# Performance work log

Measured on AMD Instinct MI355X. Metric: run time of the kernel, lower is better.

Reference implementation:

```python
import jax, jax.numpy as jnp
import numpy as np

B, T, R, NS = 16, 2048, 256, 4


def setup_inputs() -> dict:
    key = jax.random.key(0)
    ks = jax.random.split(key, 11)
    s = 1.0 / np.sqrt(R)
    inp = {
        "q": jax.random.normal(ks[0], (B, T, R), jnp.float32),
        "k": jax.random.normal(ks[1], (B, T, R), jnp.float32),
        "v": jax.random.normal(ks[2], (B, T, R), jnp.float32),
        "wq": jax.random.uniform(ks[3], (R, R), jnp.float32, -s, s),
        "bq": jax.random.uniform(ks[4], (R,), jnp.float32, -s, s),
        "wk": jax.random.uniform(ks[5], (R, R), jnp.float32, -s, s),
        "bk": jax.random.uniform(ks[6], (R,), jnp.float32, -s, s),
        "wv": jax.random.uniform(ks[7], (NS, R, R), jnp.float32, -s, s),
        "bv": jax.random.uniform(ks[8], (NS, R), jnp.float32, -s, s),
        "wp": jax.random.uniform(ks[9], (R,), jnp.float32, -s, s),
        "bp": jax.random.uniform(ks[10], (), jnp.float32, -s, s),
    }
    return inp


def reference(q, k, v, wq, bq, wk, bk, wv, bv, wp, bp):
    # linear projections (torch Linear: x @ W.T + b)
    qp = q @ wq.T + bq                                   # [B,T,R]
    kp = k @ wk.T + bk                                   # [B,T,R]
    # n_state value projections, stacked on dim 1 -> [B,NS,T,R]
    vs = jnp.einsum('btr,nor->bnto', v, wv) + bv[None, :, None, :]

    # scaled dot-product attention with tril + (score==0 -> -10000) mask quirk
    scale = 1.0 / jnp.sqrt(jnp.asarray(q.shape[-1], qp.dtype))
    score = jnp.einsum('btr,bsr->bts', qp, kp) * scale   # [B,T,T]
    score = jnp.tril(score)
    score = jnp.where(score == 0, jnp.asarray(-10000.0, score.dtype), score)
    attn = jax.nn.softmax(score, axis=-1)                # [B,T,T]

    # batched AV (original does a python loop over batch; same math)
    out = jnp.einsum('bts,bnsr->bntr', attn, vs)         # [B,NS,T,R]

    # similarity loss: 0.5 * sum |cov(proj_score[b])| averaged over batch
    proj = jnp.einsum('bntr,r->bnt', vs, wp) + bp        # [B,NS,T]

    def cov_abs_sum(X):  # X: [NS, T], rows = variables
        Xc = X - X.mean(axis=1, keepdims=True)
        c = (Xc @ Xc.T) / (X.shape[1] - 1)               # [NS,NS]
        return 0.5 * jnp.sum(jnp.abs(c))

    sim_loss = jnp.mean(jax.vmap(cov_abs_sum)(proj))
    return out, sim_loss
```

## Files before the change

kernel.cpp:

```cpp
#include <hip/hip_runtime.h>

#define B_  16
#define T_  2048
#define R_  256
#define NS_ 4

typedef unsigned short u16;
typedef __attribute__((ext_vector_type(8))) __bf16 bf16x8;
typedef __attribute__((ext_vector_type(4))) float f32x4;

__device__ __forceinline__ u16 f2bf(float f){
  union { float f; unsigned u; } x; x.f = f;
  unsigned r = x.u + 0x7FFFu + ((x.u >> 16) & 1u);
  return (u16)(r >> 16);
}
__device__ __forceinline__ float bf2f(u16 h){
  union { unsigned u; float f; } x; x.u = ((unsigned)h) << 16; return x.f;
}

__device__ __forceinline__ void async_cp16(const void* g, void* l){
  __builtin_amdgcn_global_load_lds((__attribute__((address_space(1))) void*)g,
                                   (__attribute__((address_space(3))) void*)l,
                                   16, 0, 0);
}

__global__ __launch_bounds__(256)
void cvt_kernel(const float* __restrict__ src, u16* __restrict__ dst, int n4){
  int i = blockIdx.x*256 + threadIdx.x;
  if (i >= n4) return;
  float4 f = ((const float4*)src)[i];
  ushort4 o;
  o.x = f2bf(f.x); o.y = f2bf(f.y); o.z = f2bf(f.z); o.w = f2bf(f.w);
  ((ushort4*)dst)[i] = o;
}

__global__ __launch_bounds__(256)
void zero_kernel(float* __restrict__ p, int n){
  int i = blockIdx.x*256 + threadIdx.x;
  if (i < n) p[i] = 0.0f;
}

__global__ __launch_bounds__(256, 2)
void gemm_nt_bias(const u16* __restrict__ A, const u16* __restrict__ Bm,
                  u16* __restrict__ C, const float* __restrict__ bias,
                  int lda, int ldb, int ldc, int K,
                  long long sAn, long long sBb, long long sCz,
                  int sBiasN, int biasMode)
{
  __shared__ __align__(16) u16 As[128*32];
  __shared__ __align__(16) u16 Bs[128*32];
  int tid = threadIdx.x;
  int lane = tid & 63, wave = tid >> 6;
  int z = blockIdx.z;
  int nIdx = z & 3, bIdx = z >> 2;
  A    += (long long)nIdx * sAn;
  Bm   += (long long)bIdx * sBb;
  C    += (long long)z * sCz;
  bias += (long long)nIdx * sBiasN;
  int mBase = blockIdx.y * 128;
  int nBase = blockIdx.x * 128;
  int wm = (wave >> 1) * 64, wn = (wave & 1) * 64;
  int quad = lane >> 4, lc = lane & 15;

  f32x4 acc[4][4];
  #pragma unroll
  for (int i=0;i<4;i++)
    #pragma unroll
    for (int j=0;j<4;j++) acc[i][j] = (f32x4){0.f,0.f,0.f,0.f};

  for (int k0=0; k0<K; k0+=32){
    #pragma unroll
    for (int r=0;r<2;r++){
      int c = r*256 + tid;
      int row = c >> 2, col = (c & 3)*8;
      async_cp16(A  + (long long)(mBase+row)*lda + k0 + col, (void*)(As + (r*256 + wave*64)*8));
      async_cp16(Bm + (long long)(nBase+row)*ldb + k0 + col, (void*)(Bs + (r*256 + wave*64)*8));
    }
    __syncthreads();
    bf16x8 af[4], bfr[4];
    #pragma unroll
    for (int i=0;i<4;i++){
      af[i]  = *(const bf16x8*)(As + (wm + i*16 + lc)*32 + quad*8);
      bfr[i] = *(const bf16x8*)(Bs + (wn + i*16 + lc)*32 + quad*8);
    }
    #pragma unroll
    for (int i=0;i<4;i++)
      #pragma unroll
      for (int j=0;j<4;j++)
        acc[i][j] = __builtin_amdgcn_mfma_f32_16x16x32_bf16(af[i], bfr[j], acc[i][j], 0,0,0);
    __syncthreads();
  }
  #pragma unroll
  for (int i=0;i<4;i++){
    #pragma unroll
    for (int j=0;j<4;j++){
      int colG = nBase + wn + j*16 + lc;
      float bc = (biasMode==0) ? bias[colG] : 0.0f;
      #pragma unroll
      for (int e=0;e<4;e++){
        int rowG = mBase + wm + i*16 + quad*4 + e;
        float val = acc[i][j][e] + ((biasMode==0) ? bc : bias[rowG]);
        C[(long long)rowG*ldc + colG] = f2bf(val);
      }
    }
  }
}

__global__ __launch_bounds__(256, 4)
void attn_kernel(const u16* __restrict__ qp, const u16* __restrict__ kp,
                 u16* __restrict__ P, float* __restrict__ lsum)
{
  __shared__ __align__(16) u16 Qs[64*32];
  __shared__ __align__(16) u16 Ks[128*32];
  int tid = threadIdx.x, lane = tid & 63, wave = tid >> 6;
  int b = blockIdx.y;
  int f = blockIdx.x;
  int t64 = 31;
  while (f >= (t64 >> 1) + 1){ f -= (t64 >> 1) + 1; t64--; }
  int sT = f;
  int tBase = t64 * 64;
  const u16* Q  = qp + ((long long)b*T_ + tBase) * R_;
  const u16* Kt = kp + (long long)b*T_*R_ + (long long)sT*128*R_;
  u16* Pb = P + (long long)b*T_*T_;
  const float scale = 0.0625f;
  int quad = lane >> 4, lc = lane & 15;
  int rowLoc = wave*16 + quad*4;

  f32x4 acc[8];
  #pragma unroll
  for (int j=0;j<8;j++) acc[j] = (f32x4){0.f,0.f,0.f,0.f};

  for (int k0=0;k0<R_;k0+=32){
    {
      int row = tid >> 2, col = (tid & 3)*8;
      async_cp16(Q + (long long)row*R_ + k0 + col, (void*)(Qs + (wave*64)*8));
    }
    #pragma unroll
    for (int r=0;r<2;r++){
      int c = r*256 + tid;
      int row = c >> 2, col = (c & 3)*8;
      async_cp16(Kt + (long long)row*R_ + k0 + col, (void*)(Ks + (r*256 + wave*64)*8));
    }
    __syncthreads();
    bf16x8 aq = *(const bf16x8*)(Qs + (wave*16 + lc)*32 + quad*8);
    #pragma unroll
    for (int j=0;j<8;j++){
      bf16x8 bk = *(const bf16x8*)(Ks + (j*16 + lc)*32 + quad*8);
      acc[j] = __builtin_amdgcn_mfma_f32_16x16x32_bf16(aq, bk, acc[j], 0,0,0);
    }
    __syncthreads();
  }

  int sCol0 = sT*128 + lc;
  #pragma unroll
  for (int e=0;e<4;e++){
    int t = tBase + rowLoc + e;
    long long ro = (long long)t * T_;
    float rs = 0.0f;
    #pragma unroll
    for (int j=0;j<8;j++){
      float v = acc[j][e]*scale;
      int s = sCol0 + j*16;
      if (s > t || v == 0.0f) v = -10000.0f;
      float p = __expf(v);
      rs += p;
      Pb[ro + s] = f2bf(p);
    }
    #pragma unroll
    for (int off=1; off<16; off<<=1)
      rs += __shfl_xor(rs, off, 64);
    if (lc == 0)
      atomicAdd(&lsum[b*T_ + t], rs);
  }
}

__global__ __launch_bounds__(256, 4)
void pv_kernel(const u16* __restrict__ P, const u16* __restrict__ VT,
               const float* __restrict__ lsum, float* __restrict__ out)
{
  __shared__ __align__(16) u16 As[128*32];
  __shared__ __align__(16) u16 Bs[128*32];
  int tid = threadIdx.x, lane = tid & 63, wave = tid >> 6;
  int f = blockIdx.x;
  int kf = f >> 3;
  int gr = (f & 7) + 8*(kf >> 3);
  int jIdx  = kf & 7;
  int b     = gr & 15;
  int tTile = 15 - (gr >> 4);
  int jBase = jIdx * 128;
  int t0 = tTile * 128;
  int K = t0 + 128;
  const u16* A  = P  + (long long)b*T_*T_ + (long long)t0*T_;
  const u16* Bm = VT + (long long)b*1024*T_ + (long long)jBase*T_;
  const float* lrow = lsum + b*T_;
  int wm = (wave>>1)*64, wn = (wave&1)*64;
  int quad = lane>>4, lc = lane&15;

  f32x4 acc[4][4];
  #pragma unroll
  for (int i=0;i<4;i++)
    #pragma unroll
    for (int j=0;j<4;j++) acc[i][j] = (f32x4){0.f,0.f,0.f,0.f};

  for (int k0=0; k0<K; k0+=32){
    #pragma unroll
    for (int r=0;r<2;r++){
      int c = r*256 + tid;
      int row = c >> 2, col = (c & 3)*8;
      async_cp16(A  + (long long)row*T_ + k0 + col, (void*)(As + (r*256 + wave*64)*8));
      async_cp16(Bm + (long long)row*T_ + k0 + col, (void*)(Bs + (r*256 + wave*64)*8));
    }
    __syncthreads();
    bf16x8 af[4], bfr[4];
    #pragma unroll
    for (int i=0;i<4;i++){
      af[i]  = *(const bf16x8*)(As + (wm + i*16 + lc)*32 + quad*8);
      bfr[i] = *(const bf16x8*)(Bs + (wn + i*16 + lc)*32 + quad*8);
    }
    #pragma unroll
    for (int i=0;i<4;i++)
      #pragma unroll
      for (int j=0;j<4;j++)
        acc[i][j] = __builtin_amdgcn_mfma_f32_16x16x32_bf16(af[i], bfr[j], acc[i][j], 0,0,0);
    __syncthreads();
  }
  #pragma unroll
  for (int i=0;i<4;i++){
    float rl[4];
    #pragma unroll
    for (int e=0;e<4;e++)
      rl[e] = __builtin_amdgcn_rcpf(lrow[t0 + wm + i*16 + quad*4 + e]);
    #pragma unroll
    for (int j=0;j<4;j++){
      int colJ = jBase + wn + j*16 + lc;
      int n = colJ >> 8, r = colJ & 255;
      #pragma unroll
      for (int e=0;e<4;e++){
        int t = t0 + wm + i*16 + quad*4 + e;
        out[(((long long)b*NS_ + n)*T_ + t)*R_ + r] = acc[i][j][e] * rl[e];
      }
    }
  }
}

__global__ __launch_bounds__(256)
void proj_kernel(const u16* __restrict__ VT, const float* __restrict__ wp,
                 const float* __restrict__ bp, float* __restrict__ proj){
  int gid = blockIdx.x*256 + threadIdx.x;
  int bn = gid >> 11, t = gid & 2047;
  const u16* base = VT + (long long)bn*R_*T_ + t;
  float acc = bp[0];
  #pragma unroll 8
  for (int o=0;o<R_;o++)
    acc = fmaf(bf2f(base[(long long)o*T_]), wp[o], acc);
  proj[gid] = acc;
}

__global__ __launch_bounds__(256)
void loss_batch_kernel(const float* __restrict__ proj, float* __restrict__ partial){
  __shared__ float red[4][14];
  int tid = threadIdx.x, lane = tid & 63, wave = tid >> 6;
  int b = blockIdx.x;
  const float* pb = proj + b*NS_*T_;
  float s[14];
  #pragma unroll
  for (int kk=0;kk<14;kk++) s[kk]=0.0f;
  for (int t=tid; t<T_; t+=256){
    float x0 = pb[0*T_+t], x1 = pb[1*T_+t], x2 = pb[2*T_+t], x3 = pb[3*T_+t];
    s[0]+=x0; s[1]+=x1; s[2]+=x2; s[3]+=x3;
    s[4]+=x0*x0; s[5]+=x1*x0; s[6]+=x1*x1; s[7]+=x2*x0; s[8]+=x2*x1;
    s[9]+=x2*x2; s[10]+=x3*x0; s[11]+=x3*x1; s[12]+=x3*x2; s[13]+=x3*x3;
  }
  #pragma unroll
  for (int kk=0;kk<14;kk++){
    #pragma unroll
    for (int off=1; off<64; off<<=1)
      s[kk] += __shfl_xor(s[kk], off, 64);
  }
  if (lane == 0){
    #pragma unroll
    for (int kk=0;kk<14;kk++) red[wave][kk] = s[kk];
  }
  __syncthreads();
  if (tid == 0){
    float tot[14];
    #pragma unroll
    for (int kk=0;kk<14;kk++)
      tot[kk] = red[0][kk] + red[1][kk] + red[2][kk] + red[3][kk];
    const float invT  = 1.0f/(float)T_;
    const float invT1 = 1.0f/(float)(T_-1);
    float csum = 0.0f;
    #pragma unroll
    for (int n=0;n<4;n++){
      #pragma unroll
      for (int m=0;m<=n;m++){
        int id = n*(n+1)/2 + m;
        float c = (tot[4+id] - tot[n]*tot[m]*invT) * invT1;
        csum += (n==m) ? fabsf(c) : 2.0f*fabsf(c);
      }
    }
    partial[b] = 0.5f*csum;
  }
}

__global__ void loss_final_kernel(const float* __restrict__ partial,
                                  float* __restrict__ simOut){
  if (threadIdx.x == 0){
    float sim = 0.0f;
    #pragma unroll
    for (int b=0;b<B_;b++) sim += partial[b];
    simOut[0] = sim * (1.0f/(float)B_);
  }
}

extern "C" void kernel_launch(void* const* d_in, const int* in_sizes, int n_in,
                              void* d_out, int out_size, void* d_ws, size_t ws_size,
                              hipStream_t stream)
{
  const float* q  = (const float*)d_in[0];
  const float* k  = (const float*)d_in[1];
  const float* v  = (const float*)d_in[2];
  const float* wq = (const float*)d_in[3];
  const float* bq = (const float*)d_in[4];
  const float* wk = (const float*)d_in[5];
  const float* bk = (const float*)d_in[6];
  const float* wv = (const float*)d_in[7];
  const float* bv = (const float*)d_in[8];
  const float* wp = (const float*)d_in[9];
  const float* bp = (const float*)d_in[10];
  float* out = (float*)d_out;

  char* ws = (char*)d_ws;
  u16* qbf   = (u16*)(ws + 0);
  u16* kbf   = (u16*)(ws + 16777216);
  u16* vbf   = (u16*)(ws + 33554432);
  u16* wqbf  = (u16*)(ws + 50331648);
  u16* wkbf  = (u16*)(ws + 50462720);
  u16* wvbf  = (u16*)(ws + 50593792);
  u16* qpbf  = (u16*)(ws + 51118080);
  u16* kpbf  = (u16*)(ws + 67895296);
  u16* vtbf  = (u16*)(ws + 84672512);
  u16* pbuf  = (u16*)(ws + 151781376);
  float* prj = (float*)(ws + 285999104);
  float* lpart = (float*)(ws + 0);
  float* lsum  = (float*)(ws + 16777216);

  cvt_kernel<<<8192,256,0,stream>>>(q,  qbf, 2097152);
  cvt_kernel<<<8192,256,0,stream>>>(k,  kbf, 2097152);
  cvt_kernel<<<8192,256,0,stream>>>(v,  vbf, 2097152);
  cvt_kernel<<<64,  256,0,stream>>>(wq, wqbf, 16384);
  cvt_kernel<<<64,  256,0,stream>>>(wk, wkbf, 16384);
  cvt_kernel<<<256, 256,0,stream>>>(wv, wvbf, 65536);

  dim3 gq(2,256,1);
  gemm_nt_bias<<<gq,256,0,stream>>>(qbf, wqbf, qpbf, bq, 256,256,256,256, 0,0,0, 0, 0);
  gemm_nt_bias<<<gq,256,0,stream>>>(kbf, wkbf, kpbf, bk, 256,256,256,256, 0,0,0, 0, 0);
  dim3 gv(16,2,64);
  gemm_nt_bias<<<gv,256,0,stream>>>(wvbf, vbf, vtbf, bv, 256,256,2048,256,
                                    65536LL, 524288LL, 524288LL, 256, 1);

  zero_kernel<<<128,256,0,stream>>>(lsum, 32768);
  dim3 ga(272,16,1);
  attn_kernel<<<ga,256,0,stream>>>(qpbf, kpbf, pbuf, lsum);

  pv_kernel<<<2048,256,0,stream>>>(pbuf, vtbf, lsum, out);

  proj_kernel<<<512,256,0,stream>>>(vtbf, wp, bp, prj);
  loss_batch_kernel<<<16,256,0,stream>>>(prj, lpart);
  loss_final_kernel<<<1,64,0,stream>>>(lpart, out + 33554432);
}
```

Before: 482.4 us.

## Rewrite PV GEMM with 256x256 tiles, swizzled LDS and software-pipelined async loads

The PV kernel moves from 128x128 tiles with 256 threads to 256x256 tiles with 512 threads. It uses a double-buffered 128KB LDS pipeline with XOR-swizzled layout, explicit vmcnt waits, barriers and setprio around MFMA bursts, so global loads overlap with compute. Because the causal K extent is now rounded up to 256-row tiles, a new pzero kernel zeroes the upper-triangle 128-column blocks of P that attn_kernel does not write. The aim is more reuse and fewer LDS bank conflicts, at the cost of an extra launch, some redundant work on the diagonal, and lower occupancy.

```diff
diff --git a/kernel.cpp b/kernel.cpp
--- a/kernel.cpp
+++ b/kernel.cpp
@@ -38,6 +38,18 @@
 void zero_kernel(float* __restrict__ p, int n){
   int i = blockIdx.x*256 + threadIdx.x;
   if (i < n) p[i] = 0.0f;
+}
+
+__global__ __launch_bounds__(256)
+void pzero_kernel(u16* __restrict__ P){
+  int blk = blockIdx.x;
+  int b = blk & 15, tT = blk >> 4;
+  long long base = (long long)b*T_*T_ + (long long)(tT*256)*T_ + (tT*256 + 128);
+  int r = threadIdx.x >> 1, h = threadIdx.x & 1;
+  u16* p = P + base + (long long)r*T_ + h*64;
+  uint4 z = {0u,0u,0u,0u};
+  #pragma unroll
+  for (int i=0;i<8;i++) ((uint4*)p)[i] = z;
 }
 
 __global__ __launch_bounds__(256, 2)
@@ -174,70 +186,143 @@
   }
 }
 
-__global__ __launch_bounds__(256, 4)
+#define MF(A,Bx,C) __builtin_amdgcn_mfma_f32_16x16x32_bf16(A,Bx,C,0,0,0)
+#define VM8 asm volatile("s_waitcnt vmcnt(8)" ::: "memory")
+#define VM4 asm volatile("s_waitcnt vmcnt(4)" ::: "memory")
+#define VM0 asm volatile("s_waitcnt vmcnt(0)" ::: "memory")
+#define NOWT ((void)0)
+#define NOSTG ((void)0)
+
+#define STAGE_A(KT,KH) do { \
+  const u16* sp_ = aG + (int)((KT)*64 + (KH)*32); \
+  u16* dp_ = (u16*)lds + (((KT)&1)*16384 + (KH)*8192 + wave*512); \
+  async_cp16(sp_ + stOff, dp_); \
+  async_cp16(sp_ + stOff + 128*2048, dp_ + 4096); \
+} while(0)
+#define STAGE_B(KT,KH) do { \
+  const u16* sp_ = bG + (int)((KT)*64 + (KH)*32); \
+  u16* dp_ = (u16*)lds + (32768 + ((KT)&1)*16384 + (KH)*8192 + wave*512); \
+  async_cp16(sp_ + stOff, dp_); \
+  async_cp16(sp_ + stOff + 128*2048, dp_ + 4096); \
+} while(0)
+
+#define LDA_F(BUF,KH,CU,TI) (*(const bf16x8*)(&lds[(BUF)*16384 + (KH)*8192 + (rbA + (CU)*64 + (TI)*16)*32 + qSw]))
+#define LDB_F(BUF,KH,JJ)    (*(const bf16x8*)(&lds[32768 + (BUF)*16384 + (KH)*8192 + (rbB + (JJ)*16)*32 + qSw]))
+
+#define PHASE(BUF,KH,CU,STG,WT) do { \
+  bf16x8 a0_ = LDA_F(BUF,KH,CU,0); \
+  bf16x8 a1_ = LDA_F(BUF,KH,CU,1); \
+  bf16x8 a2_ = LDA_F(BUF,KH,CU,2); \
+  bf16x8 a3_ = LDA_F(BUF,KH,CU,3); \
+  if ((CU)==0){ bF0 = LDB_F(BUF,KH,0); bF1 = LDB_F(BUF,KH,1); \
+                bF2 = LDB_F(BUF,KH,2); bF3 = LDB_F(BUF,KH,3); } \
+  STG; \
+  asm volatile("" ::: "memory"); \
+  __builtin_amdgcn_s_barrier(); \
+  asm volatile("s_waitcnt lgkmcnt(0)" ::: "memory"); \
+  __builtin_amdgcn_sched_barrier(0); \
+  __builtin_amdgcn_s_setprio(1); \
+  acc[(CU)*4+0][0]=MF(a0_,bF0,acc[(CU)*4+0][0]); \
+  acc[(CU)*4+0][1]=MF(a0_,bF1,acc[(CU)*4+0][1]); \
+  acc[(CU)*4+0][2]=MF(a0_,bF2,acc[(CU)*4+0][2]); \
+  acc[(CU)*4+0][3]=MF(a0_,bF3,acc[(CU)*4+0][3]); \
+  acc[(CU)*4+1][0]=MF(a1_,bF0,acc[(CU)*4+1][0]); \
+  acc[(CU)*4+1][1]=MF(a1_,bF1,acc[(CU)*4+1][1]); \
+  acc[(CU)*4+1][2]=MF(a1_,bF2,acc[(CU)*4+1][2]); \
+  acc[(CU)*4+1][3]=MF(a1_,bF3,acc[(CU)*4+1][3]); \
+  acc[(CU)*4+2][0]=MF(a2_,bF0,acc[(CU)*4+2][0]); \
+  acc[(CU)*4+2][1]=MF(a2_,bF1,acc[(CU)*4+2][1]); \
+  acc[(CU)*4+2][2]=MF(a2_,bF2,acc[(CU)*4+2][2]); \
+  acc[(CU)*4+2][3]=MF(a2_,bF3,acc[(CU)*4+2][3]); \
+  acc[(CU)*4+3][0]=MF(a3_,bF0,acc[(CU)*4+3][0]); \
+  acc[(CU)*4+3][1]=MF(a3_,bF1,acc[(CU)*4+3][1]); \
+  acc[(CU)*4+3][2]=MF(a3_,bF2,acc[(CU)*4+3][2]); \
+  acc[(CU)*4+3][3]=MF(a3_,bF3,acc[(CU)*4+3][3]); \
+  __builtin_amdgcn_s_setprio(0); \
+  WT; \
+  asm volatile("" ::: "memory"); \
+  __builtin_amdgcn_s_barrier(); \
+} while(0)
+
+__global__ __launch_bounds__(512, 2)
 void pv_kernel(const u16* __restrict__ P, const u16* __restrict__ VT,
                const float* __restrict__ lsum, float* __restrict__ out)
 {
-  __shared__ __align__(16) u16 As[128*32];
-  __shared__ __align__(16) u16 Bs[128*32];
+  __shared__ __align__(16) u16 lds[65536];
   int tid = threadIdx.x, lane = tid & 63, wave = tid >> 6;
   int f = blockIdx.x;
-  int kf = f >> 3;
-  int gr = (f & 7) + 8*(kf >> 3);
-  int jIdx  = kf & 7;
-  int b     = gr & 15;
-  int tTile = 15 - (gr >> 4);
-  int jBase = jIdx * 128;
-  int t0 = tTile * 128;
-  int K = t0 + 128;
-  const u16* A  = P  + (long long)b*T_*T_ + (long long)t0*T_;
-  const u16* Bm = VT + (long long)b*1024*T_ + (long long)jBase*T_;
+  int xcd = f & 7, s = f >> 3;
+  int g = xcd + 8*(s >> 2);
+  int jIdx = s & 3;
+  int b = g & 15;
+  int tT = 7 - (g >> 4);
+  int t0abs = tT * 256;
+  int nIt = 2*(tT + 1);
+
+  const u16* aG = P  + (long long)b*T_*T_ + (long long)t0abs*T_;
+  const u16* bG = VT + (long long)b*1024*T_ + (long long)(jIdx*256)*T_;
+
+  int stRow = tid >> 2;
+  int vSt = (stRow & 3) ^ ((stRow >> 2) & 3);
+  int stOff = stRow*2048 + (((tid & 3) ^ vSt) << 3);
+
+  int quad = lane >> 4, lc = lane & 15;
+  int wm = wave >> 2, wn = wave & 3;
+  int vlc = (lc & 3) ^ ((lc >> 2) & 3);
+  int qSw = ((quad ^ vlc) << 3);
+  int rbA = wm*128 + lc;
+  int rbB = wn*64 + lc;
+
+  f32x4 acc[8][4];
+  #pragma unroll
+  for (int i=0;i<8;i++)
+    #pragma unroll
+    for (int j=0;j<4;j++) acc[i][j] = (f32x4){0.f,0.f,0.f,0.f};
+  bf16x8 bF0, bF1, bF2, bF3;
+
+  STAGE_A(0,0); STAGE_B(0,0);
+  STAGE_A(0,1); STAGE_B(0,1);
+  STAGE_A(1,0); STAGE_B(1,0);
+  VM8;
+  __builtin_amdgcn_s_barrier();
+
+  for (int j = 0; j < nIt-1; ++j){
+    int k1 = 2*j+1, k2 = 2*j+2, k3 = 2*j+3;
+    PHASE(0,0,0, STAGE_A(k1,1), NOWT);
+    PHASE(0,0,1, STAGE_B(k1,1), VM8);
+    PHASE(0,1,0, STAGE_A(k2,0), NOWT);
+    PHASE(0,1,1, STAGE_B(k2,0), VM8);
+    PHASE(1,0,0, STAGE_A(k2,1), NOWT);
+    PHASE(1,0,1, STAGE_B(k2,1), VM8);
+    PHASE(1,1,0, STAGE_A(k3,0), NOWT);
+    PHASE(1,1,1, STAGE_B(k3,0), VM8);
+  }
+  {
+    int kL = 2*nIt - 1;
+    PHASE(0,0,0, STAGE_A(kL,1), NOWT);
+    PHASE(0,0,1, STAGE_B(kL,1), VM8);
+    PHASE(0,1,0, NOSTG, NOWT);
+    PHASE(0,1,1, NOSTG, VM4);
+    PHASE(1,0,0, NOSTG, NOWT);
+    PHASE(1,0,1, NOSTG, VM0);
+    PHASE(1,1,0, NOSTG, NOWT);
+    PHASE(1,1,1, NOSTG, NOWT);
+  }
+
   const float* lrow = lsum + b*T_;
-  int wm = (wave>>1)*64, wn = (wave&1)*64;
-  int quad = lane>>4, lc = lane&15;
-
-  f32x4 acc[4][4];
-  #pragma unroll
-  for (int i=0;i<4;i++)
-    #pragma unroll
-    for (int j=0;j<4;j++) acc[i][j] = (f32x4){0.f,0.f,0.f,0.f};
-
-  for (int k0=0; k0<K; k0+=32){
-    #pragma unroll
-    for (int r=0;r<2;r++){
-      int c = r*256 + tid;
-      int row = c >> 2, col = (c & 3)*8;
-      async_cp16(A  + (long long)row*T_ + k0 + col, (void*)(As + (r*256 + wave*64)*8));
-      async_cp16(Bm + (long long)row*T_ + k0 + col, (void*)(Bs + (r*256 + wave*64)*8));
-    }
-    __syncthreads();
-    bf16x8 af[4], bfr[4];
-    #pragma unroll
-    for (int i=0;i<4;i++){
-      af[i]  = *(const bf16x8*)(As + (wm + i*16 + lc)*32 + quad*8);
-      bfr[i] = *(const bf16x8*)(Bs + (wn + i*16 + lc)*32 + quad*8);
-    }
-    #pragma unroll
-    for (int i=0;i<4;i++)
-      #pragma unroll
-      for (int j=0;j<4;j++)
-        acc[i][j] = __builtin_amdgcn_mfma_f32_16x16x32_bf16(af[i], bfr[j], acc[i][j], 0,0,0);
-    __syncthreads();
-  }
-  #pragma unroll
-  for (int i=0;i<4;i++){
+  #pragma unroll
+  for (int i=0;i<8;i++){
     float rl[4];
     #pragma unroll
     for (int e=0;e<4;e++)
-      rl[e] = __builtin_amdgcn_rcpf(lrow[t0 + wm + i*16 + quad*4 + e]);
-    #pragma unroll
-    for (int j=0;j<4;j++){
-      int colJ = jBase + wn + j*16 + lc;
-      int n = colJ >> 8, r = colJ & 255;
+      rl[e] = __builtin_amdgcn_rcpf(lrow[t0abs + wm*128 + i*16 + quad*4 + e]);
+    #pragma unroll
+    for (int j2=0;j2<4;j2++){
+      int rcol = wn*64 + j2*16 + lc;
       #pragma unroll
       for (int e=0;e<4;e++){
-        int t = t0 + wm + i*16 + quad*4 + e;
-        out[(((long long)b*NS_ + n)*T_ + t)*R_ + r] = acc[i][j][e] * rl[e];
+        int t = t0abs + wm*128 + i*16 + quad*4 + e;
+        out[(((long long)b*NS_ + jIdx)*T_ + t)*R_ + rcol] = acc[i][j2][e] * rl[e];
       }
     }
   }
@@ -360,10 +445,11 @@
                                     65536LL, 524288LL, 524288LL, 256, 1);
 
   zero_kernel<<<128,256,0,stream>>>(lsum, 32768);
+  pzero_kernel<<<128,256,0,stream>>>(pbuf);
   dim3 ga(272,16,1);
   attn_kernel<<<ga,256,0,stream>>>(qpbf, kpbf, pbuf, lsum);
 
-  pv_kernel<<<2048,256,0,stream>>>(pbuf, vtbf, lsum, out);
+  pv_kernel<<<512,512,0,stream>>>(pbuf, vtbf, lsum, out);
 
   proj_kernel<<<512,256,0,stream>>>(vtbf, wp, bp, prj);
   loss_batch_kernel<<<16,256,0,stream>>>(prj, lpart);
```

New measurement: 474.9 us. No clear change (-1.5%).
